# Kernel optimization log

Measured on AMD Instinct MI355X. Metric: run time of the kernel, lower is better.

## Reference

```python
import jax, jax.numpy as jnp
import numpy as np

B, C_IN, C_OUT, H, W = 32, 64, 64, 128, 128
K, KH, KW = 4, 3, 3
HID = max(8, C_IN // 4)  # reduction=4 -> 16


def setup_inputs() -> dict:
    key = jax.random.key(0)
    ks = jax.random.split(key, 16)
    s = lambda k, shape, scale=0.1: jax.random.normal(k, shape, dtype=jnp.float32) * scale
    inp = {
        "x": jax.random.normal(ks[0], (B, C_IN, H, W), dtype=jnp.float32),
        "weight": s(ks[1], (K, C_OUT, C_IN, KH, KW)),  # static weight bank
        "bias": s(ks[2], (C_OUT,)),
        "mlp_w": s(ks[3], (HID, C_IN)),
        "mlp_b": s(ks[4], (HID,)),
        "wK": s(ks[5], (K, HID)),  "bK": s(ks[6], (K,)),
        "wO": s(ks[7], (C_OUT, HID)), "bO": s(ks[8], (C_OUT,)),
        "wI": s(ks[9], (C_IN, HID)),  "bI": s(ks[10], (C_IN,)),
        "wH": s(ks[11], (KH, HID)),   "bH": s(ks[12], (KH,)),
        "wW": s(ks[13], (KW, HID)),   "bW": s(ks[14], (KW,)),
    }
    return inp


def reference(x, weight, bias, mlp_w, mlp_b, wK, bK, wO, bO, wI, bI, wH, bH, wW, bW):
    # ---- attention branch: global avg pool -> MLP -> 5 heads ----
    g = jnp.mean(x, axis=(2, 3))                         # [B, C_in]
    h = jax.nn.relu(g @ mlp_w.T + mlp_b)                 # [B, HID]
    aK = jax.nn.softmax(h @ wK.T + bK, axis=1)           # [B, K]
    aO = jax.nn.sigmoid(h @ wO.T + bO)                   # [B, O]
    aI = jax.nn.sigmoid(h @ wI.T + bI)                   # [B, I]
    aH = jax.nn.sigmoid(h @ wH.T + bH)                   # [B, kh]
    aW = jax.nn.sigmoid(h @ wW.T + bW)                   # [B, kw]
    aH = aH / (jnp.sum(aH, axis=1, keepdims=True) + 1e-6)
    aW = aW / (jnp.sum(aW, axis=1, keepdims=True) + 1e-6)
    # fused 5-way outer product + reduction over K (same math as alpha einsum)
    w_dyn = jnp.einsum('bk,bo,bi,bh,bw,koihw->boihw', aK, aO, aI, aH, aW, weight)
    # ---- per-sample conv2d (groups=B trick expressed as vmap) ----
    def conv_one(xb, wb):
        return jax.lax.conv_general_dilated(
            xb[None], wb, window_strides=(1, 1), padding=((1, 1), (1, 1)),
            dimension_numbers=('NCHW', 'OIHW', 'NCHW'))[0]
    out = jax.vmap(conv_one)(x, w_dyn) + bias[None, :, None, None]
    return out
```

## Files before the change

kernel.cpp:

```cpp
#include <hip/hip_runtime.h>
#include <hip/hip_bf16.h>
#include <math.h>

#define BB 32
#define CI 64
#define CO 64
#define HH 128
#define WW 128
#define KK 4
#define HID 16

typedef __attribute__((ext_vector_type(8)))  __bf16 bf16x8;
typedef __attribute__((ext_vector_type(16))) float  floatx16;

__device__ __forceinline__ unsigned short f2bf(float f) {
    union { float f; unsigned int u; } a; a.f = f;
    unsigned int u = a.u;
    unsigned int r = (u + 0x7fffu + ((u >> 16) & 1u)) >> 16;
    return (unsigned short)r;
}

__global__ __launch_bounds__(256) void pooltr_kernel(const float* __restrict__ x,
                                                     float* __restrict__ rowsum,
                                                     unsigned short* __restrict__ xT) {
    const int y = blockIdx.x;
    const int b = blockIdx.y;
    const int t = threadIdx.x;
    __shared__ __align__(16) unsigned int sT[128 * 36];

    const int ic2 = t >> 3;
    const int q   = t & 7;

    const float* xb = x + ((size_t)(b * CI + 2 * ic2) * HH + y) * WW;
    const float4* r0 = reinterpret_cast<const float4*>(xb);
    const float4* r1 = reinterpret_cast<const float4*>(xb + HH * WW);
    float s0 = 0.f, s1 = 0.f;
#pragma unroll
    for (int it = 0; it < 4; it++) {
        int c4 = q + it * 8;
        float4 f0 = r0[c4];
        float4 f1 = r1[c4];
        s0 += f0.x + f0.y + f0.z + f0.w;
        s1 += f1.x + f1.y + f1.z + f1.w;
        int cb = c4 * 4;
        sT[(cb + 0) * 36 + ic2] = (unsigned)f2bf(f0.x) | ((unsigned)f2bf(f1.x) << 16);
        sT[(cb + 1) * 36 + ic2] = (unsigned)f2bf(f0.y) | ((unsigned)f2bf(f1.y) << 16);
        sT[(cb + 2) * 36 + ic2] = (unsigned)f2bf(f0.z) | ((unsigned)f2bf(f1.z) << 16);
        sT[(cb + 3) * 36 + ic2] = (unsigned)f2bf(f0.w) | ((unsigned)f2bf(f1.w) << 16);
    }
    s0 += __shfl_xor(s0, 1, 64); s1 += __shfl_xor(s1, 1, 64);
    s0 += __shfl_xor(s0, 2, 64); s1 += __shfl_xor(s1, 2, 64);
    s0 += __shfl_xor(s0, 4, 64); s1 += __shfl_xor(s1, 4, 64);
    if (q == 0) {
        *reinterpret_cast<float2*>(rowsum + ((size_t)b * HH + y) * CI + 2 * ic2) =
            make_float2(s0, s1);
    }
    __syncthreads();
#pragma unroll
    for (int jt = 0; jt < 4; jt++) {
        int idx = t + 256 * jt;
        int p   = idx >> 8;
        int r   = idx & 255;
        int c   = r >> 1;
        int h   = r & 1;
        uint4* dst = reinterpret_cast<uint4*>(
            xT + (((size_t)(b * 4 + p) * HH + y) * WW + c) * 16 + h * 8);
        *dst = *reinterpret_cast<uint4*>(&sT[c * 36 + p * 8 + h * 4]);
    }
}

__global__ __launch_bounds__(256) void attn_kernel(
    const float* __restrict__ rowsum,
    const float* __restrict__ mlp_w, const float* __restrict__ mlp_b,
    const float* __restrict__ wK, const float* __restrict__ bK,
    const float* __restrict__ wO, const float* __restrict__ bO,
    const float* __restrict__ wI, const float* __restrict__ bI,
    const float* __restrict__ wH, const float* __restrict__ bH,
    const float* __restrict__ wW, const float* __restrict__ bW,
    float* __restrict__ aK, float* __restrict__ aO, float* __restrict__ aI,
    float* __restrict__ aH, float* __restrict__ aW) {
    int b = blockIdx.x;
    int t = threadIdx.x;
    __shared__ float red[4][CI];
    __shared__ float sg[CI];
    __shared__ float sh[HID];
    __shared__ float sK[KK];
    __shared__ float sH[3];
    __shared__ float sW[3];

    {
        int ic = t & 63, seg = t >> 6;
        const float* rs = rowsum + (size_t)b * (HH * CI) + seg * 32 * CI + ic;
        float s = 0.f;
        for (int yy = 0; yy < 32; yy++) s += rs[yy * CI];
        red[seg][ic] = s;
    }
    __syncthreads();
    if (t < CI) sg[t] = (red[0][t] + red[1][t] + red[2][t] + red[3][t]) * (1.0f / (HH * WW));
    __syncthreads();

    if (t < HID) {
        float s = mlp_b[t];
        for (int c = 0; c < CI; c++) s = fmaf(mlp_w[t * CI + c], sg[c], s);
        sh[t] = fmaxf(s, 0.f);
    }
    __syncthreads();

    if (t < CO) {
        float sO = bO[t], sI = bI[t];
        for (int j = 0; j < HID; j++) {
            float hv = sh[j];
            sO = fmaf(wO[t * HID + j], hv, sO);
            sI = fmaf(wI[t * HID + j], hv, sI);
        }
        aO[b * CO + t] = 1.f / (1.f + expf(-sO));
        aI[b * CI + t] = 1.f / (1.f + expf(-sI));
    }
    if (t >= 64 && t < 64 + KK) {
        int u = t - 64;
        float s = bK[u];
        for (int j = 0; j < HID; j++) s = fmaf(wK[u * HID + j], sh[j], s);
        sK[u] = s;
    }
    if (t >= 128 && t < 131) {
        int u = t - 128;
        float s = bH[u];
        for (int j = 0; j < HID; j++) s = fmaf(wH[u * HID + j], sh[j], s);
        sH[u] = 1.f / (1.f + expf(-s));
        float s2 = bW[u];
        for (int j = 0; j < HID; j++) s2 = fmaf(wW[u * HID + j], sh[j], s2);
        sW[u] = 1.f / (1.f + expf(-s2));
    }
    __syncthreads();

    if (t == 0) {
        float m = fmaxf(fmaxf(sK[0], sK[1]), fmaxf(sK[2], sK[3]));
        float e0 = expf(sK[0] - m), e1 = expf(sK[1] - m);
        float e2 = expf(sK[2] - m), e3 = expf(sK[3] - m);
        float s = e0 + e1 + e2 + e3;
        aK[b * KK + 0] = e0 / s;
        aK[b * KK + 1] = e1 / s;
        aK[b * KK + 2] = e2 / s;
        aK[b * KK + 3] = e3 / s;
        float hs = sH[0] + sH[1] + sH[2] + 1e-6f;
        float wsum = sW[0] + sW[1] + sW[2] + 1e-6f;
        for (int i = 0; i < 3; i++) {
            aH[b * 3 + i] = sH[i] / hs;
            aW[b * 3 + i] = sW[i] / wsum;
        }
    }
}

#define WD_TOT (BB * 9 * CO * CI)
__global__ __launch_bounds__(256) void wdyn_kernel(
    const float* __restrict__ weight,
    const float* __restrict__ aK, const float* __restrict__ aO,
    const float* __restrict__ aI, const float* __restrict__ aH,
    const float* __restrict__ aW, unsigned short* __restrict__ wdbf) {
    int idx = blockIdx.x * 256 + threadIdx.x;
    if (idx >= WD_TOT) return;
    int i   = idx & 63;
    int o   = (idx >> 6) & 63;
    int bt  = idx >> 12;
    int tap = bt % 9;
    int b   = bt / 9;

    int wbase = (o * CI + i) * 9 + tap;
    const float* ak = aK + b * KK;
    float s = 0.f;
#pragma unroll
    for (int k = 0; k < KK; k++) s = fmaf(ak[k], weight[k * (CO * CI * 9) + wbase], s);
    float v = s * aO[b * CO + o] * aI[b * CI + i] *
              aH[b * 3 + tap / 3] * aW[b * 3 + tap % 3];
    int ch = i >> 4, icw = i & 15;
    wdbf[(((size_t)(b * 4 + ch) * 9 + tap) * CO + o) * 16 + icw] = f2bf(v);
}

#define ICCH 16
#define PADI 24
#define SX_ELE (6 * 130 * PADI)
#define SW_ELE (9 * 64 * PADI)
#define NXLD (6 * 130 * 2)
#define NWLD (9 * 64 * 2)
#define XPLANE (HH * WW * 16)
#define WPLANE (9 * 64 * 16)

__global__ __launch_bounds__(512, 4) void conv_kernel(
    const unsigned short* __restrict__ xT, const unsigned short* __restrict__ wdbf,
    const float* __restrict__ bias, float* __restrict__ out) {
    const int y0 = blockIdx.x * 4;
    const int b  = blockIdx.y;
    const int t  = threadIdx.x;
    const int lane = t & 63;
    const int w    = t >> 6;
    const int ry   = w >> 1;
    const int c0   = (w & 1) * 64;
    const int l31  = lane & 31;
    const int koct = lane >> 5;

    __shared__ __align__(16) unsigned short sx[SX_ELE];
    __shared__ __align__(16) unsigned short sw[SW_ELE];

    floatx16 acc[2][2];
#pragma unroll
    for (int i = 0; i < 2; i++)
#pragma unroll
        for (int j = 0; j < 2; j++)
#pragma unroll
            for (int q = 0; q < 16; q++) acc[i][j][q] = 0.f;

    const unsigned short* xb  = xT + (size_t)b * (4 * XPLANE);
    const unsigned short* wdb = wdbf + (size_t)b * (4 * WPLANE);

    int xoff[4];
    int sxoff[4];
#pragma unroll
    for (int j = 0; j < 4; j++) {
        int idx = t + 512 * j;
        xoff[j] = -1; sxoff[j] = 0;
        if (idx < NXLD) {
            int half = idx & 1, pix = idx >> 1;
            int r = pix / 130, c = pix - r * 130;
            int gy = y0 - 1 + r, gx = c - 1;
            sxoff[j] = pix * PADI + half * 8;
            if ((unsigned)gy < (unsigned)HH && (unsigned)gx < (unsigned)WW)
                xoff[j] = (gy * WW + gx) * 16 + half * 8;
        }
    }
    int woff[3], swoff[3];
#pragma unroll
    for (int j = 0; j < 3; j++) {
        int idx = t + 512 * j;
        woff[j] = 0; swoff[j] = 0;
        if (idx < NWLD) {
            int k8 = idx & 1, oi = idx >> 1;
            woff[j]  = oi * 16 + k8 * 8;
            swoff[j] = oi * PADI + k8 * 8;
        }
    }

    uint4 vx[4], vw[3];
    auto issue = [&](int chunk) {
        const unsigned short* xp = xb + (size_t)chunk * XPLANE;
        const unsigned short* wp = wdb + (size_t)chunk * WPLANE;
#pragma unroll
        for (int j = 0; j < 4; j++) {
            vx[j] = make_uint4(0u, 0u, 0u, 0u);
            if (xoff[j] >= 0)
                vx[j] = *reinterpret_cast<const uint4*>(xp + xoff[j]);
        }
#pragma unroll
        for (int j = 0; j < 3; j++) {
            if (t + 512 * j < NWLD)
                vw[j] = *reinterpret_cast<const uint4*>(wp + woff[j]);
        }
    };
    auto commit = [&]() {
#pragma unroll
        for (int j = 0; j < 4; j++)
            if (t + 512 * j < NXLD)
                *reinterpret_cast<uint4*>(&sx[sxoff[j]]) = vx[j];
#pragma unroll
        for (int j = 0; j < 3; j++)
            if (t + 512 * j < NWLD)
                *reinterpret_cast<uint4*>(&sw[swoff[j]]) = vw[j];
    };

    const int pA0 = (0 * 32 + l31) * PADI + koct * 8;
    const int pA1 = (1 * 32 + l31) * PADI + koct * 8;
    const int pB0 = (ry * 130 + c0 + 0  + l31) * PADI + koct * 8;
    const int pB1 = (ry * 130 + c0 + 32 + l31) * PADI + koct * 8;

    issue(0);
    for (int chunk = 0; chunk < 4; chunk++) {
        __syncthreads();
        commit();
        __syncthreads();
        if (chunk < 3) issue(chunk + 1);

#pragma unroll
        for (int kh = 0; kh < 3; kh++) {
#pragma unroll
            for (int kw = 0; kw < 3; kw++) {
                const int tap  = kh * 3 + kw;
                const int aoff = tap * (64 * PADI);
                const int boff = (kh * 130 + kw) * PADI;
                bf16x8 a0 = *reinterpret_cast<const bf16x8*>(&sw[pA0 + aoff]);
                bf16x8 a1 = *reinterpret_cast<const bf16x8*>(&sw[pA1 + aoff]);
                bf16x8 b0 = *reinterpret_cast<const bf16x8*>(&sx[pB0 + boff]);
                bf16x8 b1 = *reinterpret_cast<const bf16x8*>(&sx[pB1 + boff]);
                acc[0][0] = __builtin_amdgcn_mfma_f32_32x32x16_bf16(a0, b0, acc[0][0], 0, 0, 0);
                acc[0][1] = __builtin_amdgcn_mfma_f32_32x32x16_bf16(a0, b1, acc[0][1], 0, 0, 0);
                acc[1][0] = __builtin_amdgcn_mfma_f32_32x32x16_bf16(a1, b0, acc[1][0], 0, 0, 0);
                acc[1][1] = __builtin_amdgcn_mfma_f32_32x32x16_bf16(a1, b1, acc[1][1], 0, 0, 0);
            }
        }
    }

    const int y = y0 + ry;
    float* ob = out + (size_t)b * CO * HH * WW + (size_t)y * WW;
#pragma unroll
    for (int mt = 0; mt < 2; mt++) {
#pragma unroll
        for (int r = 0; r < 16; r++) {
            int oc = mt * 32 + (r & 3) + 8 * (r >> 2) + 4 * koct;
            float bv = bias[oc];
            ob[(size_t)oc * (HH * WW) + c0 + l31]      = acc[mt][0][r] + bv;
            ob[(size_t)oc * (HH * WW) + c0 + l31 + 32] = acc[mt][1][r] + bv;
        }
    }
}

extern "C" void kernel_launch(void* const* d_in, const int* in_sizes, int n_in,
                              void* d_out, int out_size, void* d_ws, size_t ws_size,
                              hipStream_t stream) {
    const float* x     = (const float*)d_in[0];
    const float* weight= (const float*)d_in[1];
    const float* bias  = (const float*)d_in[2];
    const float* mlp_w = (const float*)d_in[3];
    const float* mlp_b = (const float*)d_in[4];
    const float* wK    = (const float*)d_in[5];
    const float* bK    = (const float*)d_in[6];
    const float* wO    = (const float*)d_in[7];
    const float* bO    = (const float*)d_in[8];
    const float* wI    = (const float*)d_in[9];
    const float* bI    = (const float*)d_in[10];
    const float* wH    = (const float*)d_in[11];
    const float* bH    = (const float*)d_in[12];
    const float* wW    = (const float*)d_in[13];
    const float* bW    = (const float*)d_in[14];
    float* out = (float*)d_out;

    float* ws = (float*)d_ws;
    float* rowsum = ws;
    float* aK = ws + 262144;
    float* aO = aK + 128;
    float* aI = aO + 2048;
    float* aH = aI + 2048;
    float* aW = aH + 96;
    unsigned short* wdbf = (unsigned short*)(ws + 266560);
    unsigned short* xT   = (unsigned short*)(ws + 856384);

    pooltr_kernel<<<dim3(HH, BB), 256, 0, stream>>>(x, rowsum, xT);
    attn_kernel<<<BB, 256, 0, stream>>>(rowsum, mlp_w, mlp_b, wK, bK, wO, bO,
                                        wI, bI, wH, bH, wW, bW, aK, aO, aI, aH, aW);
    wdyn_kernel<<<(WD_TOT + 255) / 256, 256, 0, stream>>>(weight, aK, aO, aI, aH, aW, wdbf);
    conv_kernel<<<dim3(HH / 4, BB), 512, 0, stream>>>(xT, wdbf, bias, out);
}
```

Measured before the change: 321.8 us.

## Store zero-padded transposed input and feed conv MFMAs straight from global memory

The pool/transpose kernel now writes the bf16 channel-chunked input into a 130x130 plane with zeroed halo rows and columns, so the conv no longer needs bounds checks. The conv kernel drops its shared-memory staging, the double-buffered issue/commit and the block barriers, and loads MFMA operands directly from global memory, relying on L1/L2 to serve the overlapping 3x3 reuse. This removes LDS traffic and synchronisation but gives up explicit reuse and prefetch, so global load latency is exposed on every tap and has to be hidden by occupancy.

```diff
diff --git a/kernel.cpp b/kernel.cpp
--- a/kernel.cpp
+++ b/kernel.cpp
@@ -12,6 +12,10 @@
 
 typedef __attribute__((ext_vector_type(8)))  __bf16 bf16x8;
 typedef __attribute__((ext_vector_type(16))) float  floatx16;
+
+#define XPLANE_P (130 * 130 * 16)
+#define XROW_P   (130 * 16)
+#define WPLANE   (9 * 64 * 16)
 
 __device__ __forceinline__ unsigned short f2bf(float f) {
     union { float f; unsigned int u; } a; a.f = f;
@@ -55,6 +59,26 @@
         *reinterpret_cast<float2*>(rowsum + ((size_t)b * HH + y) * CI + 2 * ic2) =
             make_float2(s0, s1);
     }
+
+    if (t < 16) {
+        int ch  = t >> 2;
+        int col = (t & 2) ? 129 : 0;
+        int h   = t & 1;
+        uint4* dst = reinterpret_cast<uint4*>(
+            xT + (size_t)(b * 4 + ch) * XPLANE_P + ((size_t)(y + 1) * 130 + col) * 16 + h * 8);
+        *dst = make_uint4(0u, 0u, 0u, 0u);
+    }
+    if (y == 0 || y == HH - 1) {
+        const size_t prow = (y == 0) ? 0 : 129;
+        for (int idx = t; idx < 4 * 260; idx += 256) {
+            int ch = idx / 260;
+            int u  = idx % 260;
+            uint4* dst = reinterpret_cast<uint4*>(
+                xT + (size_t)(b * 4 + ch) * XPLANE_P + prow * XROW_P) + u;
+            *dst = make_uint4(0u, 0u, 0u, 0u);
+        }
+    }
+
     __syncthreads();
 #pragma unroll
     for (int jt = 0; jt < 4; jt++) {
@@ -64,7 +88,7 @@
         int c   = r >> 1;
         int h   = r & 1;
         uint4* dst = reinterpret_cast<uint4*>(
-            xT + (((size_t)(b * 4 + p) * HH + y) * WW + c) * 16 + h * 8);
+            xT + (size_t)(b * 4 + p) * XPLANE_P + ((size_t)(y + 1) * 130 + (c + 1)) * 16 + h * 8);
         *dst = *reinterpret_cast<uint4*>(&sT[c * 36 + p * 8 + h * 4]);
     }
 }
@@ -176,15 +200,6 @@
     wdbf[(((size_t)(b * 4 + ch) * 9 + tap) * CO + o) * 16 + icw] = f2bf(v);
 }
 
-#define ICCH 16
-#define PADI 24
-#define SX_ELE (6 * 130 * PADI)
-#define SW_ELE (9 * 64 * PADI)
-#define NXLD (6 * 130 * 2)
-#define NWLD (9 * 64 * 2)
-#define XPLANE (HH * WW * 16)
-#define WPLANE (9 * 64 * 16)
-
 __global__ __launch_bounds__(512, 4) void conv_kernel(
     const unsigned short* __restrict__ xT, const unsigned short* __restrict__ wdbf,
     const float* __restrict__ bias, float* __restrict__ out) {
@@ -198,9 +213,6 @@
     const int l31  = lane & 31;
     const int koct = lane >> 5;
 
-    __shared__ __align__(16) unsigned short sx[SX_ELE];
-    __shared__ __align__(16) unsigned short sw[SW_ELE];
-
     floatx16 acc[2][2];
 #pragma unroll
     for (int i = 0; i < 2; i++)
@@ -209,86 +221,25 @@
 #pragma unroll
             for (int q = 0; q < 16; q++) acc[i][j][q] = 0.f;
 
-    const unsigned short* xb  = xT + (size_t)b * (4 * XPLANE);
-    const unsigned short* wdb = wdbf + (size_t)b * (4 * WPLANE);
-
-    int xoff[4];
-    int sxoff[4];
-#pragma unroll
-    for (int j = 0; j < 4; j++) {
-        int idx = t + 512 * j;
-        xoff[j] = -1; sxoff[j] = 0;
-        if (idx < NXLD) {
-            int half = idx & 1, pix = idx >> 1;
-            int r = pix / 130, c = pix - r * 130;
-            int gy = y0 - 1 + r, gx = c - 1;
-            sxoff[j] = pix * PADI + half * 8;
-            if ((unsigned)gy < (unsigned)HH && (unsigned)gx < (unsigned)WW)
-                xoff[j] = (gy * WW + gx) * 16 + half * 8;
-        }
-    }
-    int woff[3], swoff[3];
-#pragma unroll
-    for (int j = 0; j < 3; j++) {
-        int idx = t + 512 * j;
-        woff[j] = 0; swoff[j] = 0;
-        if (idx < NWLD) {
-            int k8 = idx & 1, oi = idx >> 1;
-            woff[j]  = oi * 16 + k8 * 8;
-            swoff[j] = oi * PADI + k8 * 8;
-        }
-    }
-
-    uint4 vx[4], vw[3];
-    auto issue = [&](int chunk) {
-        const unsigned short* xp = xb + (size_t)chunk * XPLANE;
-        const unsigned short* wp = wdb + (size_t)chunk * WPLANE;
-#pragma unroll
-        for (int j = 0; j < 4; j++) {
-            vx[j] = make_uint4(0u, 0u, 0u, 0u);
-            if (xoff[j] >= 0)
-                vx[j] = *reinterpret_cast<const uint4*>(xp + xoff[j]);
-        }
-#pragma unroll
-        for (int j = 0; j < 3; j++) {
-            if (t + 512 * j < NWLD)
-                vw[j] = *reinterpret_cast<const uint4*>(wp + woff[j]);
-        }
-    };
-    auto commit = [&]() {
-#pragma unroll
-        for (int j = 0; j < 4; j++)
-            if (t + 512 * j < NXLD)
-                *reinterpret_cast<uint4*>(&sx[sxoff[j]]) = vx[j];
-#pragma unroll
-        for (int j = 0; j < 3; j++)
-            if (t + 512 * j < NWLD)
-                *reinterpret_cast<uint4*>(&sw[swoff[j]]) = vw[j];
-    };
-
-    const int pA0 = (0 * 32 + l31) * PADI + koct * 8;
-    const int pA1 = (1 * 32 + l31) * PADI + koct * 8;
-    const int pB0 = (ry * 130 + c0 + 0  + l31) * PADI + koct * 8;
-    const int pB1 = (ry * 130 + c0 + 32 + l31) * PADI + koct * 8;
-
-    issue(0);
-    for (int chunk = 0; chunk < 4; chunk++) {
-        __syncthreads();
-        commit();
-        __syncthreads();
-        if (chunk < 3) issue(chunk + 1);
-
+    const unsigned short* xb = xT + (size_t)b * (4 * XPLANE_P);
+    const unsigned short* wb = wdbf + (size_t)b * (4 * WPLANE);
+
+    const int aoff = l31 * 16 + koct * 8;
+    const int xoff = (c0 + l31) * 16 + koct * 8;
+
+    for (int ch = 0; ch < 4; ch++) {
+        const unsigned short* xp = xb + (size_t)ch * XPLANE_P;
+        const unsigned short* wp = wb + (size_t)ch * WPLANE;
 #pragma unroll
         for (int kh = 0; kh < 3; kh++) {
+            const unsigned short* xrow = xp + (size_t)(y0 + ry + kh) * XROW_P + xoff;
 #pragma unroll
             for (int kw = 0; kw < 3; kw++) {
-                const int tap  = kh * 3 + kw;
-                const int aoff = tap * (64 * PADI);
-                const int boff = (kh * 130 + kw) * PADI;
-                bf16x8 a0 = *reinterpret_cast<const bf16x8*>(&sw[pA0 + aoff]);
-                bf16x8 a1 = *reinterpret_cast<const bf16x8*>(&sw[pA1 + aoff]);
-                bf16x8 b0 = *reinterpret_cast<const bf16x8*>(&sx[pB0 + boff]);
-                bf16x8 b1 = *reinterpret_cast<const bf16x8*>(&sx[pB1 + boff]);
+                const unsigned short* wt = wp + (kh * 3 + kw) * 1024;
+                bf16x8 a0 = *reinterpret_cast<const bf16x8*>(wt + aoff);
+                bf16x8 a1 = *reinterpret_cast<const bf16x8*>(wt + aoff + 512);
+                bf16x8 b0 = *reinterpret_cast<const bf16x8*>(xrow + kw * 16);
+                bf16x8 b1 = *reinterpret_cast<const bf16x8*>(xrow + kw * 16 + 512);
                 acc[0][0] = __builtin_amdgcn_mfma_f32_32x32x16_bf16(a0, b0, acc[0][0], 0, 0, 0);
                 acc[0][1] = __builtin_amdgcn_mfma_f32_32x32x16_bf16(a0, b1, acc[0][1], 0, 0, 0);
                 acc[1][0] = __builtin_amdgcn_mfma_f32_32x32x16_bf16(a1, b0, acc[1][0], 0, 0, 0);
```

Measured after the change: 331.2 us. 1.03x slower.
